# Kernel optimization log

Measured on AMD Instinct MI355X. Metric: run time of the kernel, lower is better.

Reference implementation:

```python
import jax, jax.numpy as jnp
import numpy as np

N, F, D, S = 40000, 20, 128, 512
DISCOUNT = 0.995      # HP.DISCOUNT_FACTOR
ECOEF = 0.1           # HP.ENTROPY_COEF
NEG = -1e30           # masked-logit fill (avoids -inf nan grads)


def setup_inputs() -> dict:
    key = jax.random.key(0)
    ks = jax.random.split(key, 16)
    features = jax.random.normal(ks[0], (N, F), dtype=jnp.float32)
    # passive-set membership at each SEL event (host-precomputed bookkeeping)
    sel_mask = jax.random.bernoulli(ks[1], 0.3, (S, N))
    sel_idx = jax.random.randint(ks[2], (S,), 0, N)
    sel_mask = sel_mask.at[jnp.arange(S), sel_idx].set(True)  # selected clause is passive
    proof = jax.random.bernoulli(ks[3], 0.02, (N,))
    good_mask = jnp.logical_and(sel_mask, proof[None, :])
    sc = 0.05
    params = {
        'W1': jax.random.normal(ks[4], (F, D), jnp.float32) * sc,
        'b1': jnp.zeros((D,), jnp.float32),
        'W2': jax.random.normal(ks[5], (D, D), jnp.float32) * sc,
        'b2': jnp.zeros((D,), jnp.float32),
        'init_key': jax.random.normal(ks[6], (D,), jnp.float32) * sc,    # initial LSTM h (the 'key')
        'init_state': jax.random.normal(ks[7], (D,), jnp.float32) * sc,  # initial LSTM c
        'Wih': jax.random.normal(ks[8], (4 * D, D), jnp.float32) * sc,
        'Whh': jax.random.normal(ks[9], (4 * D, D), jnp.float32) * sc,
        'bih': jnp.zeros((4 * D,), jnp.float32),
        'bhh': jnp.zeros((4 * D,), jnp.float32),
    }
    return {'features': features, 'sel_mask': sel_mask, 'good_mask': good_mask,
            'sel_idx': sel_idx, **params}


def reference(features, sel_mask, good_mask, sel_idx,
              W1, b1, W2, b2, init_key, init_state, Wih, Whh, bih, bhh):
    # clause_embedder: MLP over all clause feature vectors
    emb = jax.nn.relu(features @ W1 + b1) @ W2 + b2  # [N, D]

    def step(carry, inp):
        h, c, cnt = carry          # LSTM hidden (= key), cell, active-step count
        mask, good, idx = inp
        logits = emb @ h                                   # [N] matvec over all clauses
        ml = jnp.where(mask, logits, NEG)                  # restrict to passive set
        lsm = ml - jax.scipy.special.logsumexp(ml)         # masked log_softmax
        n_pass = jnp.sum(mask).astype(lsm.dtype)
        n_good = jnp.sum(good).astype(lsm.dtype)
        n_bad = n_pass - n_good
        active = jnp.logical_and(n_good > 0, n_bad > 0)
        # mean-reduced cross-entropy over proof clauses (USE_MIN_FOR_LOSS_REDUCE=False)
        ce = -jnp.sum(jnp.where(good, lsm, 0.0)) / jnp.maximum(n_good, 1.0)
        factor = DISCOUNT ** cnt
        term = jnp.where(active, factor * (n_bad / n_pass) * ce, 0.0)
        # normalized negative entropy: dot(exp(lsm), lsm) / log(len(passive))
        minus_ent = jnp.sum(jnp.where(mask, jnp.exp(lsm) * lsm, 0.0)) \
            / jnp.log(jnp.maximum(n_pass, 2.0))
        term = term + jnp.where(active, ECOEF * minus_ent, 0.0)
        # LSTM cell update with the selected clause's embedding (torch gate order i,f,g,o)
        x = emb[idx]
        gates = Wih @ x + bih + Whh @ h + bhh
        i, f, g, o = jnp.split(gates, 4)
        c2 = jax.nn.sigmoid(f) * c + jax.nn.sigmoid(i) * jnp.tanh(g)
        h2 = jax.nn.sigmoid(o) * jnp.tanh(c2)
        return (h2, c2, cnt + active.astype(cnt.dtype)), term

    carry0 = (init_key, init_state, jnp.zeros((), features.dtype))
    (_, _, steps), terms = jax.lax.scan(step, carry0, (sel_mask, good_mask, sel_idx))
    loss = jnp.sum(terms) / jnp.maximum(steps, 1.0)
    return loss.reshape(1)
```

## Files before the change

### kernel.cpp

```cpp
#include <hip/hip_runtime.h>
#include <stdint.h>

#define N_CL 40000
#define NF   20
#define DD   128
#define SS   512
#define NW   625
#define PARTN (NW * SS)
#define NEGF (-3.0e38f)
#define DISCOUNT 0.995f
#define ECOEF 0.1f

typedef __attribute__((ext_vector_type(4))) float f32x4;
typedef __attribute__((ext_vector_type(16))) float f32x16;
typedef __attribute__((ext_vector_type(8))) short short8;
typedef __attribute__((ext_vector_type(4))) unsigned short us4;

__device__ __forceinline__ float rcpf(float x) { return __builtin_amdgcn_rcpf(x); }
__device__ __forceinline__ float sigm(float x) { return rcpf(1.f + __expf(-x)); }
__device__ __forceinline__ float tanh_fast(float x) { return 1.f - 2.f * rcpf(1.f + __expf(2.f * x)); }
__device__ __forceinline__ unsigned short f2bf(float f) {
    unsigned u = __float_as_uint(f);
    return (unsigned short)((u + 0x7fffu + ((u >> 16) & 1u)) >> 16);
}
__device__ __forceinline__ float bf2f(unsigned short s) {
    return __uint_as_float(((unsigned)s) << 16);
}

#define EMB_FMA(RR) { f32x4 hvv = *(const f32x4*)&hs[rg * 8 + RR][q]; \
    acc##RR += wv0 * hvv.x + wv1 * hvv.y + wv2 * hvv.z + wv3 * hvv.w; }
#define EMB_ST(RR) { f32x4 f = acc##RR + bv; us4 hi, lo; \
    hi[0] = f2bf(f.x); lo[0] = f2bf(f.x - bf2f(hi[0])); \
    hi[1] = f2bf(f.y); lo[1] = f2bf(f.y - bf2f(hi[1])); \
    hi[2] = f2bf(f.z); lo[2] = f2bf(f.z - bf2f(hi[2])); \
    hi[3] = f2bf(f.w); lo[3] = f2bf(f.w - bf2f(hi[3])); \
    int row_ = rbase + rg * 8 + RR; \
    *(us4*)&emb_hi[row_ * DD + c4 * 4] = hi; \
    *(us4*)&emb_lo[row_ * DD + c4 * 4] = lo; }

__global__ __launch_bounds__(256) void k_emb(const float* __restrict__ feat,
                                             const float* __restrict__ W1,
                                             const float* __restrict__ b1,
                                             const float* __restrict__ W2,
                                             const float* __restrict__ b2,
                                             unsigned short* __restrict__ emb_hi,
                                             unsigned short* __restrict__ emb_lo) {
    __shared__ float fs[64][NF];
    __shared__ float hs[64][132];
    int t = threadIdx.x;
    int rbase = blockIdx.x * 64;
    for (int i = t; i < 64 * NF; i += 256)
        fs[i / NF][i % NF] = feat[rbase * NF + i];
    __syncthreads();
    {
        int c = t & 127;
        float bb = b1[c];
#pragma unroll
        for (int k = 0; k < 32; ++k) {
            int r = (t >> 7) + 2 * k;
            float acc = bb;
#pragma unroll
            for (int f = 0; f < NF; ++f) acc += fs[r][f] * W1[f * DD + c];
            hs[r][c] = fmaxf(acc, 0.f);
        }
    }
    __syncthreads();
    int c4 = t & 31, rg = t >> 5;
    f32x4 acc0{0,0,0,0}, acc1{0,0,0,0}, acc2{0,0,0,0}, acc3{0,0,0,0},
          acc4{0,0,0,0}, acc5{0,0,0,0}, acc6{0,0,0,0}, acc7{0,0,0,0};
    for (int q = 0; q < DD; q += 4) {
        f32x4 wv0 = *(const f32x4*)&W2[(q + 0) * DD + c4 * 4];
        f32x4 wv1 = *(const f32x4*)&W2[(q + 1) * DD + c4 * 4];
        f32x4 wv2 = *(const f32x4*)&W2[(q + 2) * DD + c4 * 4];
        f32x4 wv3 = *(const f32x4*)&W2[(q + 3) * DD + c4 * 4];
        EMB_FMA(0) EMB_FMA(1) EMB_FMA(2) EMB_FMA(3)
        EMB_FMA(4) EMB_FMA(5) EMB_FMA(6) EMB_FMA(7)
    }
    f32x4 bv = *(const f32x4*)&b2[c4 * 4];
    EMB_ST(0) EMB_ST(1) EMB_ST(2) EMB_ST(3)
    EMB_ST(4) EMB_ST(5) EMB_ST(6) EMB_ST(7)
}

__global__ __launch_bounds__(256) void k_pgemm(const unsigned short* __restrict__ emb_hi,
                                               const unsigned short* __restrict__ emb_lo,
                                               const int* __restrict__ sel_idx,
                                               const float* __restrict__ Wih,
                                               const float* __restrict__ bih,
                                               const float* __restrict__ bhh,
                                               float* __restrict__ P2) {
    __shared__ __align__(16) float x8[8][DD];
    int t = threadIdx.x;
    int sb = blockIdx.x * 8;
    for (int i = t; i < 8 * DD; i += 256) {
        int sl = i >> 7, k = i & 127;
        int idx = sel_idx[sb + sl] * DD + k;
        x8[sl][k] = bf2f(emb_hi[idx]) + bf2f(emb_lo[idx]);
    }
    __syncthreads();
    for (int jj = t; jj < 512; jj += 256) {
        float base = bih[jj] + bhh[jj];
        float acc[8];
#pragma unroll
        for (int s8 = 0; s8 < 8; ++s8) acc[s8] = base;
        const float4* wr = (const float4*)(Wih + jj * DD);
        for (int q = 0; q < 32; ++q) {
            float4 w4 = wr[q];
#pragma unroll
            for (int s8 = 0; s8 < 8; ++s8) {
                const float4* xs = (const float4*)&x8[s8][0];
                float4 xv = xs[q];
                acc[s8] += w4.x * xv.x + w4.y * xv.y + w4.z * xv.z + w4.w * xv.w;
            }
        }
        int pos = jj & 127, g = jj >> 7;
        for (int s8 = 0; s8 < 8; ++s8) P2[(sb + s8) * 512 + pos * 4 + g] = acc[s8];
    }
}

#define MQ(Q,hA,hB,hC,hD) { \
    a0.x += w0##Q.x * hA; a0.y += w0##Q.y * hB; a0.z += w0##Q.z * hC; a0.w += w0##Q.w * hD; \
    a1.x += w1##Q.x * hA; a1.y += w1##Q.y * hB; a1.z += w1##Q.z * hC; a1.w += w1##Q.w * hD; \
    a2.x += w2##Q.x * hA; a2.y += w2##Q.y * hB; a2.z += w2##Q.z * hC; a2.w += w2##Q.w * hD; \
    a3.x += w3##Q.x * hA; a3.y += w3##Q.y * hB; a3.z += w3##Q.z * hC; a3.w += w3##Q.w * hD; }

#define RLD(k) float hq##k = __uint_as_float((unsigned)__builtin_amdgcn_readlane((int)hhu, k));

#define WLD(W, P) asm volatile("global_load_dwordx4 %0, %1, off" : "=v"(W) : "v"(P) : "memory")

#define STEP(J, PV) { \
    unsigned hhu = __float_as_uint(hh); \
    RLD(0)  RLD(1)  RLD(2)  RLD(3)  RLD(4)  RLD(5)  RLD(6)  RLD(7) \
    RLD(8)  RLD(9)  RLD(10) RLD(11) RLD(12) RLD(13) RLD(14) RLD(15) \
    RLD(16) RLD(17) RLD(18) RLD(19) RLD(20) RLD(21) RLD(22) RLD(23) \
    RLD(24) RLD(25) RLD(26) RLD(27) RLD(28) RLD(29) RLD(30) RLD(31) \
    if (whi) {                                   \
        int s_ = g8 * 8 + (J); \
        unsigned short ah_ = f2bf(hh); \
        unsigned short al_ = f2bf(hh - bf2f(ah_)); \
        Hhi[s_ * DD + t_el] = ah_; \
        Hlo[s_ * DD + t_el] = al_; \
    } \
    f32x4 a0{0,0,0,0}, a1{0,0,0,0}, a2{0,0,0,0}, a3{0,0,0,0}; \
    MQ(0,hq0,hq1,hq2,hq3)     MQ(1,hq4,hq5,hq6,hq7) \
    MQ(2,hq8,hq9,hq10,hq11)   MQ(3,hq12,hq13,hq14,hq15) \
    MQ(4,hq16,hq17,hq18,hq19) MQ(5,hq20,hq21,hq22,hq23) \
    MQ(6,hq24,hq25,hq26,hq27) MQ(7,hq28,hq29,hq30,hq31) \
    f32x4 ps; \
    ps.x = (a0.x + a0.y) + (a0.z + a0.w); \
    ps.y = (a1.x + a1.y) + (a1.z + a1.w); \
    ps.z = (a2.x + a2.y) + (a2.z + a2.w); \
    ps.w = (a3.x + a3.y) + (a3.z + a3.w); \
    *(f32x4*)&psum[(J) & 1][kq][gbase] = ps; \
    asm volatile("s_waitcnt lgkmcnt(0)\n\ts_barrier" ::: "memory"); \
    float q00 = psum[(J) & 1][0][t_el],       q01 = psum[(J) & 1][1][t_el]; \
    float q02 = psum[(J) & 1][2][t_el],       q03 = psum[(J) & 1][3][t_el]; \
    float q10 = psum[(J) & 1][0][128 + t_el], q11 = psum[(J) & 1][1][128 + t_el]; \
    float q12 = psum[(J) & 1][2][128 + t_el], q13 = psum[(J) & 1][3][128 + t_el]; \
    float q20 = psum[(J) & 1][0][256 + t_el], q21 = psum[(J) & 1][1][256 + t_el]; \
    float q22 = psum[(J) & 1][2][256 + t_el], q23 = psum[(J) & 1][3][256 + t_el]; \
    float q30 = psum[(J) & 1][0][384 + t_el], q31 = psum[(J) & 1][1][384 + t_el]; \
    float q32 = psum[(J) & 1][2][384 + t_el], q33 = psum[(J) & 1][3][384 + t_el]; \
    float gi = ((q00 + q01) + (q02 + q03)) + (PV).x; \
    float gf = ((q10 + q11) + (q12 + q13)) + (PV).y; \
    float gg = ((q20 + q21) + (q22 + q23)) + (PV).z; \
    float go = ((q30 + q31) + (q32 + q33)) + (PV).w; \
    float ii = sigm(gi), ff = sigm(gf), tg = tanh_fast(gg), oo = sigm(go); \
    c = ff * c + ii * tg; \
    hh = oo * tanh_fast(c); \
}

__global__ __launch_bounds__(512, 1) void k_lstm(const float* __restrict__ Whh,
                                                 const float* __restrict__ P2,
                                                 const float* __restrict__ init_h,
                                                 const float* __restrict__ init_c,
                                                 unsigned short* __restrict__ Hhi,
                                                 unsigned short* __restrict__ Hlo,
                                                 const int* __restrict__ sel,
                                                 const int* __restrict__ good,
                                                 unsigned long long* __restrict__ selw,
                                                 unsigned long long* __restrict__ goodw) {
    if (blockIdx.x != 0) {
        int wave = ((blockIdx.x - 1) * 512 + threadIdx.x) >> 6;
        int lane = threadIdx.x & 63;
        for (int i = 0; i < 64; ++i) {
            int chunk = wave * 64 + i;
            int s = chunk / NW;
            int b = chunk - s * NW;
            int idx = s * N_CL + b * 64 + lane;
            unsigned long long bs = __ballot(sel[idx]  != 0);
            unsigned long long bg = __ballot(good[idx] != 0);
            if (lane == 0) { selw[b * SS + s] = bs; goodw[b * SS + s] = bg; }
        }
        return;
    }

    __shared__ __align__(16) float psum[2][4][512];

    int t = threadIdx.x, w = t >> 6, l = t & 63;
    int kq = w & 3, gh = w >> 2, ln = l & 31;
    int gbase = gh * 256 + l * 4;
    int t_el = kq * 32 + ln;
    bool whi = (gh == 1) && (l >= 32);

    const f32x4* wr0 = (const f32x4*)(Whh + (gbase + 0) * DD + kq * 32);
    const f32x4* wr1 = (const f32x4*)(Whh + (gbase + 1) * DD + kq * 32);
    const f32x4* wr2 = (const f32x4*)(Whh + (gbase + 2) * DD + kq * 32);
    const f32x4* wr3 = (const f32x4*)(Whh + (gbase + 3) * DD + kq * 32);
    f32x4 w00, w01, w02, w03, w04, w05, w06, w07;
    f32x4 w10, w11, w12, w13, w14, w15, w16, w17;
    f32x4 w20, w21, w22, w23, w24, w25, w26, w27;
    f32x4 w30, w31, w32, w33, w34, w35, w36, w37;
    WLD(w00, wr0 + 0); WLD(w01, wr0 + 1); WLD(w02, wr0 + 2); WLD(w03, wr0 + 3);
    WLD(w04, wr0 + 4); WLD(w05, wr0 + 5); WLD(w06, wr0 + 6); WLD(w07, wr0 + 7);
    WLD(w10, wr1 + 0); WLD(w11, wr1 + 1); WLD(w12, wr1 + 2); WLD(w13, wr1 + 3);
    WLD(w14, wr1 + 4); WLD(w15, wr1 + 5); WLD(w16, wr1 + 6); WLD(w17, wr1 + 7);
    WLD(w20, wr2 + 0); WLD(w21, wr2 + 1); WLD(w22, wr2 + 2); WLD(w23, wr2 + 3);
    WLD(w24, wr2 + 4); WLD(w25, wr2 + 5); WLD(w26, wr2 + 6); WLD(w27, wr2 + 7);
    WLD(w30, wr3 + 0); WLD(w31, wr3 + 1); WLD(w32, wr3 + 2); WLD(w33, wr3 + 3);
    WLD(w34, wr3 + 4); WLD(w35, wr3 + 5); WLD(w36, wr3 + 6); WLD(w37, wr3 + 7);
    asm volatile("s_waitcnt vmcnt(0)" ::: "memory");
    __builtin_amdgcn_sched_barrier(0);

    float c  = init_c[t_el];
    float hh = init_h[t_el];

    for (int g8 = 0; g8 < 64; ++g8) {
        const float* pb = P2 + g8 * 4096 + t_el * 4;
        f32x4 pv0 = *(const f32x4*)(pb + 0 * 512);
        f32x4 pv1 = *(const f32x4*)(pb + 1 * 512);
        f32x4 pv2 = *(const f32x4*)(pb + 2 * 512);
        f32x4 pv3 = *(const f32x4*)(pb + 3 * 512);
        STEP(0, pv0) STEP(1, pv1) STEP(2, pv2) STEP(3, pv3)
        f32x4 pv4 = *(const f32x4*)(pb + 4 * 512);
        f32x4 pv5 = *(const f32x4*)(pb + 5 * 512);
        f32x4 pv6 = *(const f32x4*)(pb + 6 * 512);
        f32x4 pv7 = *(const f32x4*)(pb + 7 * 512);
        STEP(4, pv4) STEP(5, pv5) STEP(6, pv6) STEP(7, pv7)
    }
}

__global__ __launch_bounds__(256, 1) void k_logits(
        const unsigned short* __restrict__ emb_hi,
        const unsigned short* __restrict__ emb_lo,
        const unsigned short* __restrict__ Hhi,
        const unsigned short* __restrict__ Hlo,
        const unsigned long long* __restrict__ selw,
        const unsigned long long* __restrict__ goodw,
        float* __restrict__ part) {
    int b = blockIdx.x;
    int t = threadIdx.x, wv = t >> 6, l = t & 63;
    int ln = l & 31, lh = l >> 5;
    int rb = b * 64;
    const short8* A0h = (const short8*)(emb_hi + (rb + ln) * DD + lh * 8);
    const short8* A0l = (const short8*)(emb_lo + (rb + ln) * DD + lh * 8);
    const short8* A1h = (const short8*)(emb_hi + (rb + 32 + ln) * DD + lh * 8);
    const short8* A1l = (const short8*)(emb_lo + (rb + 32 + ln) * DD + lh * 8);
    for (int sg = 0; sg < 4; ++sg) {
        int s0 = sg * 128 + wv * 32;
        const short8* Bhp = (const short8*)(Hhi + (s0 + ln) * DD + lh * 8);
        const short8* Blp = (const short8*)(Hlo + (s0 + ln) * DD + lh * 8);
        f32x16 acc0, acc1;
#pragma unroll
        for (int r = 0; r < 16; ++r) { acc0[r] = 0.f; acc1[r] = 0.f; }
#pragma unroll
        for (int kc = 0; kc < 8; ++kc) {
            short8 a0h = A0h[kc * 2], a0l = A0l[kc * 2];
            short8 a1h = A1h[kc * 2], a1l = A1l[kc * 2];
            short8 bh = Bhp[kc * 2], bl = Blp[kc * 2];
            acc0 = __builtin_amdgcn_mfma_f32_32x32x16_bf16(a0h, bh, acc0, 0, 0, 0);
            acc0 = __builtin_amdgcn_mfma_f32_32x32x16_bf16(a0l, bh, acc0, 0, 0, 0);
            acc0 = __builtin_amdgcn_mfma_f32_32x32x16_bf16(a0h, bl, acc0, 0, 0, 0);
            acc1 = __builtin_amdgcn_mfma_f32_32x32x16_bf16(a1h, bh, acc1, 0, 0, 0);
            acc1 = __builtin_amdgcn_mfma_f32_32x32x16_bf16(a1l, bh, acc1, 0, 0, 0);
            acc1 = __builtin_amdgcn_mfma_f32_32x32x16_bf16(a1h, bl, acc1, 0, 0, 0);
        }
        int s = s0 + ln;
        unsigned long long sw = selw[b * SS + s];
        unsigned long long gw = goodw[b * SS + s];
        float m = NEGF;
#pragma unroll
        for (int r = 0; r < 16; ++r) {
            int row = (r & 3) + 8 * (r >> 2) + 4 * lh;
            float v0 = acc0[r], v1 = acc1[r];
            m = fmaxf(m, ((sw >> row) & 1ull) ? v0 : NEGF);
            m = fmaxf(m, ((sw >> (row + 32)) & 1ull) ? v1 : NEGF);
        }
        m = fmaxf(m, __shfl_xor(m, 32));
        float se = 0.f, sl = 0.f, slg = 0.f;
#pragma unroll
        for (int r = 0; r < 16; ++r) {
            int row = (r & 3) + 8 * (r >> 2) + 4 * lh;
            float v0 = acc0[r], v1 = acc1[r];
            float e0 = ((sw >> row) & 1ull) ? __expf(v0 - m) : 0.f;
            float e1 = ((sw >> (row + 32)) & 1ull) ? __expf(v1 - m) : 0.f;
            se += e0 + e1;
            sl += e0 * v0 + e1 * v1;
            slg += (((gw >> row) & 1ull) ? v0 : 0.f)
                 + (((gw >> (row + 32)) & 1ull) ? v1 : 0.f);
        }
        se += __shfl_xor(se, 32);
        sl += __shfl_xor(sl, 32);
        slg += __shfl_xor(slg, 32);
        if (lh == 0) {
            int o = s * NW + b;
            part[0 * PARTN + o] = m;
            part[1 * PARTN + o] = se;
            part[2 * PARTN + o] = sl;
            part[3 * PARTN + o] = slg;
            part[4 * PARTN + o] = (float)__popcll(sw);
            part[5 * PARTN + o] = (float)__popcll(gw);
        }
    }
}

__global__ __launch_bounds__(64) void k_reduce(const float* __restrict__ part,
                                               float* __restrict__ Aout,
                                               float* __restrict__ Bout,
                                               float* __restrict__ actout) {
    int s = blockIdx.x;
    int t = threadIdx.x;
    float m = NEGF, se = 0.f, sl = 0.f, slg = 0.f, np = 0.f, ng = 0.f;
    for (int b = t; b < NW; b += 64) {
        int o = s * NW + b;
        float m2  = part[0 * PARTN + o];
        float se2 = part[1 * PARTN + o];
        float sl2 = part[2 * PARTN + o];
        slg += part[3 * PARTN + o];
        np  += part[4 * PARTN + o];
        ng  += part[5 * PARTN + o];
        float nm = fmaxf(m, m2);
        float a = __expf(m - nm), a2 = __expf(m2 - nm);
        se = se * a + se2 * a2;
        sl = sl * a + sl2 * a2;
        m = nm;
    }
    for (int off = 32; off > 0; off >>= 1) {
        float m2  = __shfl_xor(m, off);
        float se2 = __shfl_xor(se, off);
        float sl2 = __shfl_xor(sl, off);
        slg += __shfl_xor(slg, off);
        np  += __shfl_xor(np, off);
        ng  += __shfl_xor(ng, off);
        float nm = fmaxf(m, m2);
        float a = __expf(m - nm), a2 = __expf(m2 - nm);
        se = se * a + se2 * a2;
        sl = sl * a + sl2 * a2;
        m = nm;
    }
    if (t == 0) {
        float lse = m + logf(se);
        float nbad = np - ng;
        int active = (ng > 0.5f) && (nbad > 0.5f);
        float ce = (ng * lse - slg) / fmaxf(ng, 1.f);
        float A = (nbad / fmaxf(np, 1.f)) * ce;
        float minus_ent = sl / se - lse;
        float B = ECOEF * (minus_ent / logf(fmaxf(np, 2.0f)));
        Aout[s] = A; Bout[s] = B; actout[s] = active ? 1.f : 0.f;
    }
}

__global__ __launch_bounds__(64) void k_final(const float* __restrict__ A,
                                              const float* __restrict__ B,
                                              const float* __restrict__ act,
                                              float* __restrict__ out) {
    int lane = threadIdx.x;
    float loss = 0.f;
    int base = 0;
    for (int ch = 0; ch < 8; ++ch) {
        int s = ch * 64 + lane;
        bool a = act[s] > 0.5f;
        unsigned long long bal = __ballot(a);
        unsigned long long ltmask = (lane == 0) ? 0ull : (~0ull >> (64 - lane));
        int pre = __popcll(bal & ltmask);
        if (a) {
            float f = powf(DISCOUNT, (float)(base + pre));
            loss += f * A[s] + B[s];
        }
        base += __popcll(bal);
    }
    for (int off = 32; off > 0; off >>= 1) loss += __shfl_xor(loss, off);
    if (lane == 0) out[0] = loss / fmaxf((float)base, 1.f);
}

extern "C" void kernel_launch(void* const* d_in, const int* in_sizes, int n_in,
                              void* d_out, int out_size, void* d_ws, size_t ws_size,
                              hipStream_t stream) {
    (void)in_sizes; (void)n_in; (void)out_size; (void)ws_size;
    const float* feat    = (const float*)d_in[0];
    const int*   sel     = (const int*)d_in[1];
    const int*   good    = (const int*)d_in[2];
    const int*   sel_idx = (const int*)d_in[3];
    const float* W1      = (const float*)d_in[4];
    const float* b1      = (const float*)d_in[5];
    const float* W2      = (const float*)d_in[6];
    const float* b2      = (const float*)d_in[7];
    const float* init_h  = (const float*)d_in[8];
    const float* init_c  = (const float*)d_in[9];
    const float* Wih     = (const float*)d_in[10];
    const float* Whh     = (const float*)d_in[11];
    const float* bih     = (const float*)d_in[12];
    const float* bhh     = (const float*)d_in[13];
    float* out = (float*)d_out;
    char* ws = (char*)d_ws;

    unsigned short* emb_hi = (unsigned short*)(ws + 20480000);
    unsigned short* emb_lo = (unsigned short*)(ws + 30720000);
    float*          P2     = (float*)(ws + 40960000);
    unsigned short* Hhi    = (unsigned short*)(ws + 42008576);
    unsigned short* Hlo    = (unsigned short*)(ws + 42139648);
    unsigned long long* selw  = (unsigned long long*)(ws + 42270720);
    unsigned long long* goodw = (unsigned long long*)(ws + 44830720);
    float*          part   = (float*)(ws + 47390720);
    float*          Aarr   = (float*)(ws + 55070720);
    float*          Barr   = (float*)(ws + 55072768);
    float*          actarr = (float*)(ws + 55074816);

    k_emb   <<<NW, 256, 0, stream>>>(feat, W1, b1, W2, b2, emb_hi, emb_lo);
    k_pgemm <<<64, 256, 0, stream>>>(emb_hi, emb_lo, sel_idx, Wih, bih, bhh, P2);
    k_lstm  <<<626, 512, 0, stream>>>(Whh, P2, init_h, init_c, Hhi, Hlo,
                                      sel, good, selw, goodw);
    k_logits<<<NW, 256, 0, stream>>>(emb_hi, emb_lo, Hhi, Hlo, selw, goodw, part);
    k_reduce<<<SS, 64, 0, stream>>>(part, Aarr, Barr, actarr);
    k_final <<<1, 64, 0, stream>>>(Aarr, Barr, actarr, out);
}
```

Baseline: 682.8 us.

## Split LSTM Whh weights between LDS and per-step global reloads instead of registers

The recurrent LSTM kernel used to hold each thread's whole 128-float slice of Whh in VGPRs. It now stages 3/8 of each slice in LDS and reloads the other 5/8 from global memory (expected to hit in cache) inside every step. The row mapping also changes so each lane owns one row per group, and the partial-sum stores become scalar writes. The goal is to cut register pressure in the serial recurrence, at the cost of extra LDS and global loads on the latency-critical 512-step chain.

```diff
diff --git a/kernel.cpp b/kernel.cpp
--- a/kernel.cpp
+++ b/kernel.cpp
@@ -117,15 +117,20 @@
     }
 }
 
-#define MQ(Q,hA,hB,hC,hD) { \
-    a0.x += w0##Q.x * hA; a0.y += w0##Q.y * hB; a0.z += w0##Q.z * hC; a0.w += w0##Q.w * hD; \
-    a1.x += w1##Q.x * hA; a1.y += w1##Q.y * hB; a1.z += w1##Q.z * hC; a1.w += w1##Q.w * hD; \
-    a2.x += w2##Q.x * hA; a2.y += w2##Q.y * hB; a2.z += w2##Q.z * hC; a2.w += w2##Q.w * hD; \
-    a3.x += w3##Q.x * hA; a3.y += w3##Q.y * hB; a3.z += w3##Q.z * hC; a3.w += w3##Q.w * hD; }
-
 #define RLD(k) float hq##k = __uint_as_float((unsigned)__builtin_amdgcn_readlane((int)hhu, k));
 
-#define WLD(W, P) asm volatile("global_load_dwordx4 %0, %1, off" : "=v"(W) : "v"(P) : "memory")
+#define FMA4(A, W, HA, HB, HC, HD) { \
+    A.x += (W).x * HA; A.y += (W).y * HB; A.z += (W).z * HC; A.w += (W).w * HD; }
+
+#define ROWFMA(A, R) { \
+    f32x4 s0_ = *(const f32x4*)&wl_sh[wbase + 0 * 1024 + 256 * (R)]; \
+    f32x4 s1_ = *(const f32x4*)&wl_sh[wbase + 1 * 1024 + 256 * (R)]; \
+    f32x4 s2_ = *(const f32x4*)&wl_sh[wbase + 2 * 1024 + 256 * (R)]; \
+    FMA4(A, s0_, hq0, hq1, hq2, hq3)    FMA4(A, s1_, hq4, hq5, hq6, hq7) \
+    FMA4(A, s2_, hq8, hq9, hq10, hq11) \
+    FMA4(A, g##R##0, hq12, hq13, hq14, hq15) FMA4(A, g##R##1, hq16, hq17, hq18, hq19) \
+    FMA4(A, g##R##2, hq20, hq21, hq22, hq23) FMA4(A, g##R##3, hq24, hq25, hq26, hq27) \
+    FMA4(A, g##R##4, hq28, hq29, hq30, hq31) }
 
 #define STEP(J, PV) { \
     unsigned hhu = __float_as_uint(hh); \
@@ -133,6 +138,10 @@
     RLD(8)  RLD(9)  RLD(10) RLD(11) RLD(12) RLD(13) RLD(14) RLD(15) \
     RLD(16) RLD(17) RLD(18) RLD(19) RLD(20) RLD(21) RLD(22) RLD(23) \
     RLD(24) RLD(25) RLD(26) RLD(27) RLD(28) RLD(29) RLD(30) RLD(31) \
+    f32x4 g00 = gW0[0], g01 = gW0[1], g02 = gW0[2], g03 = gW0[3], g04 = gW0[4]; \
+    f32x4 g10 = gW1[0], g11 = gW1[1], g12 = gW1[2], g13 = gW1[3], g14 = gW1[4]; \
+    f32x4 g20 = gW2[0], g21 = gW2[1], g22 = gW2[2], g23 = gW2[3], g24 = gW2[4]; \
+    f32x4 g30 = gW3[0], g31 = gW3[1], g32 = gW3[2], g33 = gW3[3], g34 = gW3[4]; \
     if (whi) {                                   \
         int s_ = g8 * 8 + (J); \
         unsigned short ah_ = f2bf(hh); \
@@ -141,16 +150,11 @@
         Hlo[s_ * DD + t_el] = al_; \
     } \
     f32x4 a0{0,0,0,0}, a1{0,0,0,0}, a2{0,0,0,0}, a3{0,0,0,0}; \
-    MQ(0,hq0,hq1,hq2,hq3)     MQ(1,hq4,hq5,hq6,hq7) \
-    MQ(2,hq8,hq9,hq10,hq11)   MQ(3,hq12,hq13,hq14,hq15) \
-    MQ(4,hq16,hq17,hq18,hq19) MQ(5,hq20,hq21,hq22,hq23) \
-    MQ(6,hq24,hq25,hq26,hq27) MQ(7,hq28,hq29,hq30,hq31) \
-    f32x4 ps; \
-    ps.x = (a0.x + a0.y) + (a0.z + a0.w); \
-    ps.y = (a1.x + a1.y) + (a1.z + a1.w); \
-    ps.z = (a2.x + a2.y) + (a2.z + a2.w); \
-    ps.w = (a3.x + a3.y) + (a3.z + a3.w); \
-    *(f32x4*)&psum[(J) & 1][kq][gbase] = ps; \
+    ROWFMA(a0, 0) ROWFMA(a1, 1) ROWFMA(a2, 2) ROWFMA(a3, 3) \
+    psum[(J) & 1][kq][prow]       = (a0.x + a0.y) + (a0.z + a0.w); \
+    psum[(J) & 1][kq][prow + 64]  = (a1.x + a1.y) + (a1.z + a1.w); \
+    psum[(J) & 1][kq][prow + 128] = (a2.x + a2.y) + (a2.z + a2.w); \
+    psum[(J) & 1][kq][prow + 192] = (a3.x + a3.y) + (a3.z + a3.w); \
     asm volatile("s_waitcnt lgkmcnt(0)\n\ts_barrier" ::: "memory"); \
     float q00 = psum[(J) & 1][0][t_el],       q01 = psum[(J) & 1][1][t_el]; \
     float q02 = psum[(J) & 1][2][t_el],       q03 = psum[(J) & 1][3][t_el]; \
@@ -195,31 +199,27 @@
     }
 
     __shared__ __align__(16) float psum[2][4][512];
+    __shared__ __align__(16) float wl_sh[24576];
 
     int t = threadIdx.x, w = t >> 6, l = t & 63;
     int kq = w & 3, gh = w >> 2, ln = l & 31;
-    int gbase = gh * 256 + l * 4;
     int t_el = kq * 32 + ln;
     bool whi = (gh == 1) && (l >= 32);
 
-    const f32x4* wr0 = (const f32x4*)(Whh + (gbase + 0) * DD + kq * 32);
-    const f32x4* wr1 = (const f32x4*)(Whh + (gbase + 1) * DD + kq * 32);
-    const f32x4* wr2 = (const f32x4*)(Whh + (gbase + 2) * DD + kq * 32);
-    const f32x4* wr3 = (const f32x4*)(Whh + (gbase + 3) * DD + kq * 32);
-    f32x4 w00, w01, w02, w03, w04, w05, w06, w07;
-    f32x4 w10, w11, w12, w13, w14, w15, w16, w17;
-    f32x4 w20, w21, w22, w23, w24, w25, w26, w27;
-    f32x4 w30, w31, w32, w33, w34, w35, w36, w37;
-    WLD(w00, wr0 + 0); WLD(w01, wr0 + 1); WLD(w02, wr0 + 2); WLD(w03, wr0 + 3);
-    WLD(w04, wr0 + 4); WLD(w05, wr0 + 5); WLD(w06, wr0 + 6); WLD(w07, wr0 + 7);
-    WLD(w10, wr1 + 0); WLD(w11, wr1 + 1); WLD(w12, wr1 + 2); WLD(w13, wr1 + 3);
-    WLD(w14, wr1 + 4); WLD(w15, wr1 + 5); WLD(w16, wr1 + 6); WLD(w17, wr1 + 7);
-    WLD(w20, wr2 + 0); WLD(w21, wr2 + 1); WLD(w22, wr2 + 2); WLD(w23, wr2 + 3);
-    WLD(w24, wr2 + 4); WLD(w25, wr2 + 5); WLD(w26, wr2 + 6); WLD(w27, wr2 + 7);
-    WLD(w30, wr3 + 0); WLD(w31, wr3 + 1); WLD(w32, wr3 + 2); WLD(w33, wr3 + 3);
-    WLD(w34, wr3 + 4); WLD(w35, wr3 + 5); WLD(w36, wr3 + 6); WLD(w37, wr3 + 7);
-    asm volatile("s_waitcnt vmcnt(0)" ::: "memory");
-    __builtin_amdgcn_sched_barrier(0);
+    for (int i = t; i < 24576; i += 512) {
+        int ww = i / 3072, rem = i - ww * 3072;
+        int qq = rem >> 10, r2 = rem & 1023;
+        int row = r2 >> 2, jj = r2 & 3;
+        wl_sh[i] = Whh[((ww >> 2) * 256 + row) * DD + (ww & 3) * 32 + qq * 4 + jj];
+    }
+    __syncthreads();
+
+    const f32x4* gW0 = (const f32x4*)(Whh + (size_t)(gh * 256 +       l) * DD + kq * 32 + 12);
+    const f32x4* gW1 = (const f32x4*)(Whh + (size_t)(gh * 256 +  64 + l) * DD + kq * 32 + 12);
+    const f32x4* gW2 = (const f32x4*)(Whh + (size_t)(gh * 256 + 128 + l) * DD + kq * 32 + 12);
+    const f32x4* gW3 = (const f32x4*)(Whh + (size_t)(gh * 256 + 192 + l) * DD + kq * 32 + 12);
+    int wbase = w * 3072 + 4 * l;
+    int prow  = gh * 256 + l;
 
     float c  = init_c[t_el];
     float hh = init_h[t_el];
```

Result: slower. 2.430 ms (+255.9%).
